# Optimization experiments

Measured on AMD Instinct MI355X. Metric: run time of the kernel, lower is better.

The kernel has to match this reference:

```python
import jax, jax.numpy as jnp
import numpy as np

N = 262144       # rows
D = 256          # feature dim
CLUSTER = 512    # number of clusters


def setup_inputs() -> dict:
    key = jax.random.key(0)
    k1, k2 = jax.random.split(key)
    matrix = jax.random.normal(k1, (N, D), dtype=jnp.float32)
    label = jax.random.randint(k2, (N,), 0, CLUSTER, dtype=jnp.int32)
    return {"matrix": matrix, "label": label}


def reference(matrix, label):
    # Segment-mean: scatter-add rows into their cluster, divide by counts.
    # (Intended math of the original per-row loop + count-normalize.)
    sums = jax.ops.segment_sum(matrix, label, num_segments=CLUSTER)            # [C, D]
    counts = jax.ops.segment_sum(
        jnp.ones((matrix.shape[0],), matrix.dtype), label, num_segments=CLUSTER
    )                                                                          # [C]
    centers = sums / jnp.maximum(counts, 1.0)[:, None]                         # [C, D]

    # torch.nn.functional.pdist: L2 distance over all unordered pairs i<j.
    iu, ju = jnp.triu_indices(CLUSTER, k=1)                                    # static [P]
    diff = centers[iu] - centers[ju]                                           # [P, D]
    sq = jnp.sum(diff * diff, axis=-1)                                         # [P]
    dist = jnp.sqrt(jnp.maximum(sq, 1e-12))                                    # eps-guard for sqrt grad
    return -jnp.mean(dist)
```

## Files before the change

kernel.cpp:

```cpp
#include <hip/hip_runtime.h>

#define NROWS   262144
#define DIM     256
#define CLUSTER 512
#define NPAIR   (CLUSTER * (CLUSTER - 1) / 2)
#define G       16
#define CPG     32
#define R       64
#define CHUNK   (NROWS / R)
#define CAP     256
#define PAIR_BLOCKS 2044

__global__ __launch_bounds__(256) void k_gather(const float* __restrict__ matrix,
                                                const int* __restrict__ label,
                                                float* __restrict__ partial,
                                                int* __restrict__ countpart) {
    int g = blockIdx.x & (G - 1);
    int r = blockIdx.x >> 4;
    int t = threadIdx.x;
    int w = t >> 6, lane = t & 63;
    int chunkStart = r * CHUNK;

    __shared__ float sums[CPG][DIM];
    __shared__ unsigned short list[4][CAP];
    __shared__ int cur[4];
    __shared__ int cnt[CPG];

    {
        float4* s4 = (float4*)&sums[0][0];
        for (int i = t; i < CPG * DIM / 4; i += 256) s4[i] = make_float4(0.f, 0.f, 0.f, 0.f);
        if (t < 4) cur[t] = 0;
        if (t < CPG) cnt[t] = 0;
    }
    __syncthreads();

    for (int i = t; i < CHUNK; i += 256) {
        int lab = label[chunkStart + i];
        if ((lab >> 5) == g) {
            int cl = lab & (CPG - 1);
            int cls = cl & 3;
            int q = cl >> 2;
            atomicAdd(&cnt[cl], 1);
            int pos = atomicAdd(&cur[cls], 1);
            if (pos < CAP) list[cls][pos] = (unsigned short)(i | (q << 12));
        }
    }
    __syncthreads();

    int m = min(cur[w], CAP);
    #pragma unroll 2
    for (int k = 0; k < m; ++k) {
        int e = list[w][k];
        int lidx = e & 0xFFF;
        int cl = ((e >> 12) << 2) | w;
        const float4* row = (const float4*)(matrix + (size_t)(chunkStart + lidx) * DIM);
        float4 v = row[lane];
        float4* dst = (float4*)&sums[cl][lane * 4];
        float4 s = *dst;
        s.x += v.x; s.y += v.y; s.z += v.z; s.w += v.w;
        *dst = s;
    }
    __syncthreads();

    const float4* s4 = (const float4*)&sums[0][0];
    #pragma unroll
    for (int f = 0; f < 8; ++f) {
        int idx = f * 256 + t;
        int cl = idx >> 6;
        int d4 = idx & 63;
        int c = g * CPG + cl;
        ((float4*)(partial + ((size_t)c * R + r) * DIM))[d4] = s4[idx];
    }
    if (t < CPG) countpart[r * CLUSTER + g * CPG + t] = cnt[t];
}

__global__ __launch_bounds__(256) void k_center(const float* __restrict__ partial,
                                                const int* __restrict__ countpart,
                                                float* __restrict__ centers) {
    int c = blockIdx.x, d = threadIdx.x;
    __shared__ float invc;
    if (d == 0) {
        int s = 0;
        for (int r = 0; r < R; ++r) s += countpart[r * CLUSTER + c];
        invc = 1.0f / (float)max(s, 1);
    }
    float acc = 0.f;
    const float* p = partial + (size_t)c * R * DIM + d;
    #pragma unroll 8
    for (int r = 0; r < R; ++r) acc += p[r * DIM];
    __syncthreads();
    centers[c * DIM + d] = acc * invc;
}

__device__ __forceinline__ long long tri_off(long long i) {
    return i * (2 * CLUSTER - i - 1) / 2;
}

__global__ __launch_bounds__(256) void k_pairs(const float* __restrict__ centers,
                                               float* __restrict__ partials) {
    int wave = threadIdx.x >> 6;
    int lane = threadIdx.x & 63;
    long long base = ((long long)blockIdx.x * 4 + wave) * 16;

    double sq = sqrt((double)((2LL * CLUSTER - 1) * (2LL * CLUSTER - 1) - 8 * base));
    int i = (int)(((2 * CLUSTER - 1) - sq) * 0.5);
    if (i < 0) i = 0;
    while (tri_off(i + 1) <= base) ++i;
    while (tri_off(i) > base) --i;
    int j = (int)(base - tri_off(i)) + i + 1;

    float wsum = 0.f;
    #pragma unroll 4
    for (int q = 0; q < 16; ++q) {
        const float4* ci = (const float4*)(centers + (size_t)i * DIM);
        const float4* cj = (const float4*)(centers + (size_t)j * DIM);
        float4 a = ci[lane], b = cj[lane];
        float dx = a.x - b.x, dy = a.y - b.y, dz = a.z - b.z, dw = a.w - b.w;
        float local = dx * dx + dy * dy + dz * dz + dw * dw;
        #pragma unroll
        for (int o = 32; o; o >>= 1) local += __shfl_xor(local, o, 64);
        wsum += sqrtf(fmaxf(local, 1e-12f));
        if (++j == CLUSTER) { ++i; j = i + 1; }
    }

    __shared__ float bsum[4];
    if (lane == 0) bsum[wave] = wsum;
    __syncthreads();
    if (threadIdx.x == 0)
        partials[blockIdx.x] = bsum[0] + bsum[1] + bsum[2] + bsum[3];
}

__global__ __launch_bounds__(256) void k_final(const float* __restrict__ partials, int nb,
                                               float* __restrict__ out) {
    __shared__ float s[256];
    float acc = 0.f;
    for (int i = threadIdx.x; i < nb; i += 256) acc += partials[i];
    s[threadIdx.x] = acc;
    __syncthreads();
    for (int d = 128; d; d >>= 1) {
        if (threadIdx.x < d) s[threadIdx.x] += s[threadIdx.x + d];
        __syncthreads();
    }
    if (threadIdx.x == 0) out[0] = -s[0] / (float)NPAIR;
}

extern "C" void kernel_launch(void* const* d_in, const int* in_sizes, int n_in,
                              void* d_out, int out_size, void* d_ws, size_t ws_size,
                              hipStream_t stream) {
    const float* matrix = (const float*)d_in[0];
    const int* label = (const int*)d_in[1];
    float* out = (float*)d_out;

    float* partial   = (float*)d_ws;
    float* centers   = partial + (size_t)CLUSTER * R * DIM;
    float* ppart     = centers + (size_t)CLUSTER * DIM;
    int*   countpart = (int*)(ppart + 4096);

    k_gather<<<G * R, 256, 0, stream>>>(matrix, label, partial, countpart);
    k_center<<<CLUSTER, 256, 0, stream>>>(partial, countpart, centers);
    k_pairs<<<PAIR_BLOCKS, 256, 0, stream>>>(centers, ppart);
    k_final<<<1, 256, 0, stream>>>(ppart, PAIR_BLOCKS, out);
}
```

Before: 400.3 us.

## Counting-sort rows by cluster and accumulate sums in registers per wave

Replaces the capped per-wave row lists and the shared-memory sum tile with a two-pass counting sort. One pass counts labels, a prefix sum builds per-cluster offsets, and a second pass fills a full-chunk index list. Each wave then walks contiguous per-cluster segments and accumulates in registers, writing each partial once. This drops the 32KB shared accumulator tile and its read-modify-write traffic, and removes the silent CAP truncation. The cost is a second read of the labels and a serial prefix computed by one thread.

```diff
diff --git a/kernel.cpp b/kernel.cpp
--- a/kernel.cpp
+++ b/kernel.cpp
@@ -8,7 +8,6 @@
 #define CPG     32
 #define R       64
 #define CHUNK   (NROWS / R)
-#define CAP     256
 #define PAIR_BLOCKS 2044
 
 __global__ __launch_bounds__(256) void k_gather(const float* __restrict__ matrix,
@@ -19,57 +18,54 @@
     int r = blockIdx.x >> 4;
     int t = threadIdx.x;
     int w = t >> 6, lane = t & 63;
-    int chunkStart = r * CHUNK;
+    int base = r * CHUNK;
 
-    __shared__ float sums[CPG][DIM];
-    __shared__ unsigned short list[4][CAP];
-    __shared__ int cur[4];
+    __shared__ unsigned short list[CHUNK];
     __shared__ int cnt[CPG];
+    __shared__ int off[CPG + 1];
+    __shared__ int cur[CPG];
 
-    {
-        float4* s4 = (float4*)&sums[0][0];
-        for (int i = t; i < CPG * DIM / 4; i += 256) s4[i] = make_float4(0.f, 0.f, 0.f, 0.f);
-        if (t < 4) cur[t] = 0;
-        if (t < CPG) cnt[t] = 0;
+    if (t < CPG) cnt[t] = 0;
+    __syncthreads();
+
+    for (int i = t; i < CHUNK; i += 256) {
+        int lab = label[base + i];
+        if ((lab >> 5) == g) atomicAdd(&cnt[lab & (CPG - 1)], 1);
+    }
+    __syncthreads();
+
+    if (t == 0) {
+        int s = 0;
+        #pragma unroll
+        for (int c = 0; c < CPG; ++c) { off[c] = s; cur[c] = s; s += cnt[c]; }
+        off[CPG] = s;
     }
     __syncthreads();
 
     for (int i = t; i < CHUNK; i += 256) {
-        int lab = label[chunkStart + i];
+        int lab = label[base + i];
         if ((lab >> 5) == g) {
-            int cl = lab & (CPG - 1);
-            int cls = cl & 3;
-            int q = cl >> 2;
-            atomicAdd(&cnt[cl], 1);
-            int pos = atomicAdd(&cur[cls], 1);
-            if (pos < CAP) list[cls][pos] = (unsigned short)(i | (q << 12));
+            int p = atomicAdd(&cur[lab & (CPG - 1)], 1);
+            list[p] = (unsigned short)i;
         }
     }
     __syncthreads();
 
-    int m = min(cur[w], CAP);
-    #pragma unroll 2
-    for (int k = 0; k < m; ++k) {
-        int e = list[w][k];
-        int lidx = e & 0xFFF;
-        int cl = ((e >> 12) << 2) | w;
-        const float4* row = (const float4*)(matrix + (size_t)(chunkStart + lidx) * DIM);
-        float4 v = row[lane];
-        float4* dst = (float4*)&sums[cl][lane * 4];
-        float4 s = *dst;
-        s.x += v.x; s.y += v.y; s.z += v.z; s.w += v.w;
-        *dst = s;
-    }
-    __syncthreads();
-
-    const float4* s4 = (const float4*)&sums[0][0];
     #pragma unroll
-    for (int f = 0; f < 8; ++f) {
-        int idx = f * 256 + t;
-        int cl = idx >> 6;
-        int d4 = idx & 63;
+    for (int q = 0; q < 8; ++q) {
+        int cl = q * 4 + w;
+        int s0 = off[cl], s1 = off[cl + 1];
+        float ax = 0.f, ay = 0.f, az = 0.f, aw = 0.f;
+        #pragma unroll 4
+        for (int k = s0; k < s1; ++k) {
+            int li = list[k];
+            const float4* row = (const float4*)(matrix + (size_t)(base + li) * DIM);
+            float4 v = row[lane];
+            ax += v.x; ay += v.y; az += v.z; aw += v.w;
+        }
         int c = g * CPG + cl;
-        ((float4*)(partial + ((size_t)c * R + r) * DIM))[d4] = s4[idx];
+        ((float4*)(partial + ((size_t)c * R + r) * DIM))[lane] =
+            make_float4(ax, ay, az, aw);
     }
     if (t < CPG) countpart[r * CLUSTER + g * CPG + t] = cnt[t];
 }
```

After: 402.0 us. Within noise of the previous version (+0.4%).
